# Optimization experiments

Hardware: AMD Instinct MI355X
Metric: run time of the kernel (lower is better)

Reference implementation:

```python
import jax, jax.numpy as jnp
import numpy as np

QMIN, QMAX = -128, 127  # int8 range

def setup_inputs() -> dict:
    key = jax.random.key(0)
    k1, k2, k3 = jax.random.split(key, 3)
    B, S, DIN, DOUT = 8, 2048, 4096, 4096
    x = jax.random.normal(k1, (B, S, DIN), dtype=jnp.float32)
    weight = jax.random.normal(k2, (DOUT, DIN), dtype=jnp.float32) * 0.02
    bias = jax.random.normal(k3, (DOUT,), dtype=jnp.float32) * 0.01
    # per-tensor asymmetric activation qparams (as produced by a calibrated observer)
    act_scale = jnp.float32(0.05)
    act_zero_point = jnp.int32(3)
    # per-output-channel symmetric weight scales (block_size = (1, in_features))
    weight_scale = jnp.max(jnp.abs(weight), axis=1) / 127.0  # [DOUT]
    return {"x": x, "weight": weight, "bias": bias,
            "act_scale": act_scale, "act_zero_point": act_zero_point,
            "weight_scale": weight_scale}

def reference(x, weight, bias, act_scale, act_zero_point, weight_scale):
    # 1) quantize activations: per-tensor asymmetric int8
    qx = jnp.clip(jnp.round(x / act_scale) + act_zero_point, QMIN, QMAX).astype(jnp.int8)
    # 2) quantize weight: per-output-channel symmetric int8 (zero_point = 0)
    qw = jnp.clip(jnp.round(weight / weight_scale[:, None]), QMIN, QMAX).astype(jnp.int8)
    acc = jnp.einsum('bsk,nk->bsn',
                     qx.astype(jnp.int32) - act_zero_point.astype(jnp.int32),
                     qw.astype(jnp.int32))  # [B, S, DOUT] int32
    # 4) dequantize: combined scale = act_scale * weight_scale[n], then bias
    out = acc.astype(jnp.float32) * (act_scale * weight_scale) + bias
    return out
```

## Files before the change

### kernel.cpp

```cpp
#include <hip/hip_runtime.h>
#include <cstdint>

#define M_DIM 16384
#define N_DIM 4096
#define K_DIM 4096

#define BM 256
#define BN 256
#define BK 128

typedef __attribute__((ext_vector_type(4))) int int32x4;
typedef __attribute__((ext_vector_type(4))) float f32x4;

#define GLLD16(g, l)                                              \
  __builtin_amdgcn_global_load_lds(                               \
      (const __attribute__((address_space(1))) void*)(g),         \
      (__attribute__((address_space(3))) void*)(l), 16, 0, 0)

__global__ void quant_x_kernel(const float* __restrict__ x,
                               const float* __restrict__ sp,
                               const int* __restrict__ zpp,
                               int8_t* __restrict__ qx) {
  const float s = sp[0];
  const int zp = zpp[0];
  const size_t b = (size_t)blockIdx.x * 1024;
  const f32x4* x4 = (const f32x4*)x;
  unsigned* q4 = (unsigned*)qx;
#pragma unroll
  for (int i = 0; i < 4; i++) {
    const size_t idx = b + (size_t)i * 256 + threadIdx.x;
    f32x4 v = __builtin_nontemporal_load(&x4[idx]);
    int q0 = min(127, max(-128, (int)rintf(v[0] / s) + zp));
    int q1 = min(127, max(-128, (int)rintf(v[1] / s) + zp));
    int q2 = min(127, max(-128, (int)rintf(v[2] / s) + zp));
    int q3 = min(127, max(-128, (int)rintf(v[3] / s) + zp));
    q4[idx] = (unsigned)(q0 & 255) | ((unsigned)(q1 & 255) << 8) |
              ((unsigned)(q2 & 255) << 16) | ((unsigned)(q3 & 255) << 24);
  }
}

__global__ void quant_w_kernel(const float* __restrict__ w,
                               const float* __restrict__ wscale,
                               const float* __restrict__ bias,
                               const float* __restrict__ sp,
                               const int* __restrict__ zpp,
                               int8_t* __restrict__ qw,
                               float* __restrict__ cs,
                               float* __restrict__ off) {
  const int n = blockIdx.x;
  const float ws = wscale[n];
  const float s = sp[0];
  const int zp = zpp[0];
  const f32x4* wr = (const f32x4*)(w + (size_t)n * K_DIM);
  unsigned* qr = (unsigned*)(qw + (size_t)n * K_DIM);
  int sum = 0;
#pragma unroll
  for (int it = 0; it < K_DIM / (256 * 4); it++) {
    const int idx = it * 256 + threadIdx.x;
    f32x4 v = __builtin_nontemporal_load(&wr[idx]);
    int q0 = min(127, max(-128, (int)rintf(v[0] / ws)));
    int q1 = min(127, max(-128, (int)rintf(v[1] / ws)));
    int q2 = min(127, max(-128, (int)rintf(v[2] / ws)));
    int q3 = min(127, max(-128, (int)rintf(v[3] / ws)));
    sum += q0 + q1 + q2 + q3;
    qr[idx] = (unsigned)(q0 & 255) | ((unsigned)(q1 & 255) << 8) |
              ((unsigned)(q2 & 255) << 16) | ((unsigned)(q3 & 255) << 24);
  }
  __shared__ int red[4];
#pragma unroll
  for (int o = 32; o > 0; o >>= 1) sum += __shfl_down(sum, o, 64);
  if ((threadIdx.x & 63) == 0) red[threadIdx.x >> 6] = sum;
  __syncthreads();
  if (threadIdx.x == 0) {
    const int tot = red[0] + red[1] + red[2] + red[3];
    const float c = s * ws;
    cs[n] = c;
    off[n] = bias[n] - (float)(zp * tot) * c;
  }
}

__global__ __launch_bounds__(512, 2) void gemm_i8(
    const int8_t* __restrict__ qx, const int8_t* __restrict__ qw,
    const float* __restrict__ cs, const float* __restrict__ off,
    float* __restrict__ out) {
  __shared__ __align__(16) int8_t lds[131072];

  const int tid = threadIdx.x;
  const int lane = tid & 63;
  const int wave = tid >> 6;
  const int wm = wave >> 2;
  const int wn = wave & 3;

  const int bid = blockIdx.x;
  const int swz = (bid & 7) * 128 + (bid >> 3);
  const int n0 = (swz & 15) * BN;
  const int m0 = (swz >> 4) * BM;

  int32x4 acc[8][4] = {};
  int32x4 af[8], bf0[4], bf1[4];

  const int scol = ((lane & 7) ^ ((lane >> 3) & 7)) * 16;
  const int8_t* pA[2][2];
  const int8_t* pB[2][2];
#pragma unroll
  for (int h = 0; h < 2; h++)
#pragma unroll
    for (int j = 0; j < 2; j++) {
      const int r = h * 128 + (wave * 2 + j) * 8 + (lane >> 3);
      const int ga = ((r >> 6) & 1) * 128 + (r >> 7) * 64 + (r & 63);
      const int gb = ((r >> 5) & 3) * 64 + (r >> 7) * 32 + (r & 31);
      pA[h][j] = qx + (size_t)(m0 + ga) * K_DIM + scol;
      pB[h][j] = qw + (size_t)(n0 + gb) * K_DIM + scol;
    }

  const int fr = lane & 15;
  const int quad = lane >> 4;
  int aoffs[8], boffs[4];
#pragma unroll
  for (int mtl = 0; mtl < 4; mtl++)
#pragma unroll
    for (int ks = 0; ks < 2; ks++) {
      const int r = wm * 64 + mtl * 16 + fr;
      const int c = (ks * 4 + quad) ^ (fr & 7);
      aoffs[mtl * 2 + ks] = r * 128 + c * 16;
    }
#pragma unroll
  for (int ntl = 0; ntl < 2; ntl++)
#pragma unroll
    for (int ks = 0; ks < 2; ks++) {
      const int r = wn * 32 + ntl * 16 + fr;
      const int c = (ks * 4 + quad) ^ (fr & 7);
      boffs[ntl * 2 + ks] = r * 128 + c * 16;
    }

#define STAGE(rbase, h, P, kb)                                          \
  do {                                                                  \
    GLLD16(P[h][0] + (kb), lds + (rbase) + (h) * 16384 + wave * 2048);  \
    GLLD16(P[h][1] + (kb),                                              \
           lds + (rbase) + (h) * 16384 + wave * 2048 + 1024);           \
  } while (0)

#define LDA(buf, h)                                                     \
  do {                                                                  \
    _Pragma("unroll") for (int q = 0; q < 8; q++) af[q] =               \
        *(const int32x4*)(lds + (buf) * 65536 + (h) * 16384 + aoffs[q]); \
  } while (0)

#define LDB(buf, g, BF)                                                 \
  do {                                                                  \
    _Pragma("unroll") for (int q = 0; q < 4; q++) BF[q] =               \
        *(const int32x4*)(lds + (buf) * 65536 + 32768 + (g) * 16384 +   \
                          boffs[q]);                                    \
  } while (0)

#define MM(h, g, BF)                                                       \
  do {                                                                    \
    _Pragma("unroll") for (int mtl = 0; mtl < 4; mtl++)                   \
        _Pragma("unroll") for (int ntl = 0; ntl < 2; ntl++) {             \
      acc[(h)*4 + mtl][(g)*2 + ntl] = __builtin_amdgcn_mfma_i32_16x16x64_i8( \
          BF[ntl * 2 + 0], af[mtl * 2 + 0], acc[(h)*4 + mtl][(g)*2 + ntl], \
          0, 0, 0);                                                        \
      acc[(h)*4 + mtl][(g)*2 + ntl] = __builtin_amdgcn_mfma_i32_16x16x64_i8( \
          BF[ntl * 2 + 1], af[mtl * 2 + 1], acc[(h)*4 + mtl][(g)*2 + ntl], \
          0, 0, 0);                                                        \
    }                                                                      \
  } while (0)

#define BAR() __builtin_amdgcn_s_barrier()
#define WAITLGKM() asm volatile("s_waitcnt lgkmcnt(0)" ::: "memory")
#define VM6() asm volatile("s_waitcnt vmcnt(6)" ::: "memory")
#define PRIO(x) __builtin_amdgcn_s_setprio(x)

  STAGE(0, 0, pA, 0);
  STAGE(0, 1, pA, 0);
  STAGE(32768, 0, pB, 0);
  STAGE(32768, 1, pB, 0);
  STAGE(65536, 0, pA, 128);
  STAGE(98304, 0, pB, 128);
  STAGE(98304, 1, pB, 128);
  VM6();
  BAR();

  for (int i = 0; i < K_DIM / (2 * BK); i++) {
    const int kb1 = ((2 * i + 1) << 7) & (K_DIM - 1);
    const int kb2 = ((2 * i + 2) << 7) & (K_DIM - 1);
    const int kb3 = ((2 * i + 3) << 7) & (K_DIM - 1);
    LDA(0, 0);
    LDB(0, 0, bf0);
    STAGE(65536, 1, pA, kb1);
    BAR(); WAITLGKM(); PRIO(1); MM(0, 0, bf0); PRIO(0); BAR();
    LDB(0, 1, bf1);
    STAGE(0, 0, pA, kb2);
    BAR(); WAITLGKM(); PRIO(1); MM(0, 1, bf1); PRIO(0); BAR();
    LDA(0, 1);
    STAGE(32768, 0, pB, kb2);
    BAR(); WAITLGKM(); PRIO(1); MM(1, 1, bf1); PRIO(0); BAR();
    STAGE(32768, 1, pB, kb2);
    VM6();
    BAR(); PRIO(1); MM(1, 0, bf0); PRIO(0); BAR();
    LDA(1, 0);
    LDB(1, 0, bf0);
    STAGE(0, 1, pA, kb2);
    BAR(); WAITLGKM(); PRIO(1); MM(0, 0, bf0); PRIO(0); BAR();
    LDB(1, 1, bf1);
    STAGE(65536, 0, pA, kb3);
    BAR(); WAITLGKM(); PRIO(1); MM(0, 1, bf1); PRIO(0); BAR();
    LDA(1, 1);
    STAGE(98304, 0, pB, kb3);
    BAR(); WAITLGKM(); PRIO(1); MM(1, 1, bf1); PRIO(0); BAR();
    STAGE(98304, 1, pB, kb3);
    VM6();
    BAR(); PRIO(1); MM(1, 0, bf0); PRIO(0); BAR();
  }

#pragma unroll
  for (int nt = 0; nt < 4; nt++) {
    const int colb = n0 + wn * 64 + nt * 16 + quad * 4;
    const f32x4 c4 = *(const f32x4*)(cs + colb);
    const f32x4 o4 = *(const f32x4*)(off + colb);
#pragma unroll
    for (int mt = 0; mt < 8; mt++) {
      const int row = m0 + wm * 128 + mt * 16 + fr;
      f32x4 v;
      v[0] = (float)acc[mt][nt][0] * c4[0] + o4[0];
      v[1] = (float)acc[mt][nt][1] * c4[1] + o4[1];
      v[2] = (float)acc[mt][nt][2] * c4[2] + o4[2];
      v[3] = (float)acc[mt][nt][3] * c4[3] + o4[3];
      __builtin_nontemporal_store(
          v, (f32x4*)(out + (size_t)row * N_DIM + colb));
    }
  }
#undef STAGE
#undef LDA
#undef LDB
#undef MM
#undef BAR
#undef WAITLGKM
#undef VM6
#undef PRIO
}

extern "C" void kernel_launch(void* const* d_in, const int* in_sizes, int n_in,
                              void* d_out, int out_size, void* d_ws,
                              size_t ws_size, hipStream_t stream) {
  const float* x = (const float*)d_in[0];
  const float* w = (const float*)d_in[1];
  const float* bias = (const float*)d_in[2];
  const float* act_scale = (const float*)d_in[3];
  const int* zp = (const int*)d_in[4];
  const float* wscale = (const float*)d_in[5];
  float* out = (float*)d_out;

  int8_t* qx = (int8_t*)d_ws;
  int8_t* qw = qx + (size_t)M_DIM * K_DIM;
  float* cs = (float*)(qw + (size_t)N_DIM * K_DIM);
  float* off = cs + N_DIM;

  quant_x_kernel<<<16384, 256, 0, stream>>>(x, act_scale, zp, qx);
  quant_w_kernel<<<N_DIM, 256, 0, stream>>>(w, wscale, bias, act_scale, zp,
                                            qw, cs, off);
  gemm_i8<<<dim3((M_DIM / BM) * (N_DIM / BN)), 512, 0, stream>>>(qx, qw, cs,
                                                                 off, out);
}
```

Baseline: 666.2 us.

## Fuse quant kernels and restructure GEMM to stream B from global

```diff
diff --git a/kernel.cpp b/kernel.cpp
--- a/kernel.cpp
+++ b/kernel.cpp
@@ -17,65 +17,64 @@
       (const __attribute__((address_space(1))) void*)(g),         \
       (__attribute__((address_space(3))) void*)(l), 16, 0, 0)
 
-__global__ void quant_x_kernel(const float* __restrict__ x,
-                               const float* __restrict__ sp,
-                               const int* __restrict__ zpp,
-                               int8_t* __restrict__ qx) {
-  const float s = sp[0];
-  const int zp = zpp[0];
-  const size_t b = (size_t)blockIdx.x * 1024;
-  const f32x4* x4 = (const f32x4*)x;
-  unsigned* q4 = (unsigned*)qx;
-#pragma unroll
-  for (int i = 0; i < 4; i++) {
-    const size_t idx = b + (size_t)i * 256 + threadIdx.x;
-    f32x4 v = __builtin_nontemporal_load(&x4[idx]);
-    int q0 = min(127, max(-128, (int)rintf(v[0] / s) + zp));
-    int q1 = min(127, max(-128, (int)rintf(v[1] / s) + zp));
-    int q2 = min(127, max(-128, (int)rintf(v[2] / s) + zp));
-    int q3 = min(127, max(-128, (int)rintf(v[3] / s) + zp));
-    q4[idx] = (unsigned)(q0 & 255) | ((unsigned)(q1 & 255) << 8) |
-              ((unsigned)(q2 & 255) << 16) | ((unsigned)(q3 & 255) << 24);
-  }
-}
-
-__global__ void quant_w_kernel(const float* __restrict__ w,
-                               const float* __restrict__ wscale,
-                               const float* __restrict__ bias,
-                               const float* __restrict__ sp,
-                               const int* __restrict__ zpp,
-                               int8_t* __restrict__ qw,
-                               float* __restrict__ cs,
-                               float* __restrict__ off) {
-  const int n = blockIdx.x;
-  const float ws = wscale[n];
-  const float s = sp[0];
-  const int zp = zpp[0];
-  const f32x4* wr = (const f32x4*)(w + (size_t)n * K_DIM);
-  unsigned* qr = (unsigned*)(qw + (size_t)n * K_DIM);
-  int sum = 0;
-#pragma unroll
-  for (int it = 0; it < K_DIM / (256 * 4); it++) {
-    const int idx = it * 256 + threadIdx.x;
-    f32x4 v = __builtin_nontemporal_load(&wr[idx]);
-    int q0 = min(127, max(-128, (int)rintf(v[0] / ws)));
-    int q1 = min(127, max(-128, (int)rintf(v[1] / ws)));
-    int q2 = min(127, max(-128, (int)rintf(v[2] / ws)));
-    int q3 = min(127, max(-128, (int)rintf(v[3] / ws)));
-    sum += q0 + q1 + q2 + q3;
-    qr[idx] = (unsigned)(q0 & 255) | ((unsigned)(q1 & 255) << 8) |
-              ((unsigned)(q2 & 255) << 16) | ((unsigned)(q3 & 255) << 24);
-  }
+__global__ void quant_fused(const float* __restrict__ x,
+                            const float* __restrict__ w,
+                            const float* __restrict__ wscale,
+                            const float* __restrict__ bias,
+                            const float* __restrict__ sp,
+                            const int* __restrict__ zpp,
+                            int8_t* __restrict__ qx,
+                            int8_t* __restrict__ qw,
+                            float* __restrict__ cs,
+                            float* __restrict__ off) {
   __shared__ int red[4];
-#pragma unroll
-  for (int o = 32; o > 0; o >>= 1) sum += __shfl_down(sum, o, 64);
-  if ((threadIdx.x & 63) == 0) red[threadIdx.x >> 6] = sum;
-  __syncthreads();
-  if (threadIdx.x == 0) {
-    const int tot = red[0] + red[1] + red[2] + red[3];
-    const float c = s * ws;
-    cs[n] = c;
-    off[n] = bias[n] - (float)(zp * tot) * c;
+  if (blockIdx.x < 16384) {
+    const float s = sp[0];
+    const int zp = zpp[0];
+    const size_t b = (size_t)blockIdx.x * 1024;
+    const f32x4* x4 = (const f32x4*)x;
+    unsigned* q4 = (unsigned*)qx;
+#pragma unroll
+    for (int i = 0; i < 4; i++) {
+      const size_t idx = b + (size_t)i * 256 + threadIdx.x;
+      f32x4 v = __builtin_nontemporal_load(&x4[idx]);
+      int q0 = min(127, max(-128, (int)rintf(v[0] / s) + zp));
+      int q1 = min(127, max(-128, (int)rintf(v[1] / s) + zp));
+      int q2 = min(127, max(-128, (int)rintf(v[2] / s) + zp));
+      int q3 = min(127, max(-128, (int)rintf(v[3] / s) + zp));
+      q4[idx] = (unsigned)(q0 & 255) | ((unsigned)(q1 & 255) << 8) |
+                ((unsigned)(q2 & 255) << 16) | ((unsigned)(q3 & 255) << 24);
+    }
+  } else {
+    const int n = blockIdx.x - 16384;
+    const float ws = wscale[n];
+    const float s = sp[0];
+    const int zp = zpp[0];
+    const f32x4* wr = (const f32x4*)(w + (size_t)n * K_DIM);
+    unsigned* qr = (unsigned*)(qw + (size_t)n * K_DIM);
+    int sum = 0;
+#pragma unroll
+    for (int it = 0; it < K_DIM / (256 * 4); it++) {
+      const int idx = it * 256 + threadIdx.x;
+      f32x4 v = __builtin_nontemporal_load(&wr[idx]);
+      int q0 = min(127, max(-128, (int)rintf(v[0] / ws)));
+      int q1 = min(127, max(-128, (int)rintf(v[1] / ws)));
+      int q2 = min(127, max(-128, (int)rintf(v[2] / ws)));
+      int q3 = min(127, max(-128, (int)rintf(v[3] / ws)));
+      sum += q0 + q1 + q2 + q3;
+      qr[idx] = (unsigned)(q0 & 255) | ((unsigned)(q1 & 255) << 8) |
+                ((unsigned)(q2 & 255) << 16) | ((unsigned)(q3 & 255) << 24);
+    }
+#pragma unroll
+    for (int o = 32; o > 0; o >>= 1) sum += __shfl_down(sum, o, 64);
+    if ((threadIdx.x & 63) == 0) red[threadIdx.x >> 6] = sum;
+    __syncthreads();
+    if (threadIdx.x == 0) {
+      const int tot = red[0] + red[1] + red[2] + red[3];
+      const float c = s * ws;
+      cs[n] = c;
+      off[n] = bias[n] - (float)(zp * tot) * c;
+    }
   }
 }
 
@@ -83,144 +82,120 @@
     const int8_t* __restrict__ qx, const int8_t* __restrict__ qw,
     const float* __restrict__ cs, const float* __restrict__ off,
     float* __restrict__ out) {
-  __shared__ __align__(16) int8_t lds[131072];
+  __shared__ __align__(16) int8_t lds[98304];
 
   const int tid = threadIdx.x;
   const int lane = tid & 63;
   const int wave = tid >> 6;
-  const int wm = wave >> 2;
-  const int wn = wave & 3;
+  const int wm = wave >> 1;
+  const int wn = wave & 1;
 
   const int bid = blockIdx.x;
   const int swz = (bid & 7) * 128 + (bid >> 3);
   const int n0 = (swz & 15) * BN;
   const int m0 = (swz >> 4) * BM;
 
-  int32x4 acc[8][4] = {};
-  int32x4 af[8], bf0[4], bf1[4];
-
-  const int scol = ((lane & 7) ^ ((lane >> 3) & 7)) * 16;
-  const int8_t* pA[2][2];
-  const int8_t* pB[2][2];
-#pragma unroll
-  for (int h = 0; h < 2; h++)
-#pragma unroll
-    for (int j = 0; j < 2; j++) {
-      const int r = h * 128 + (wave * 2 + j) * 8 + (lane >> 3);
-      const int ga = ((r >> 6) & 1) * 128 + (r >> 7) * 64 + (r & 63);
-      const int gb = ((r >> 5) & 3) * 64 + (r >> 7) * 32 + (r & 31);
-      pA[h][j] = qx + (size_t)(m0 + ga) * K_DIM + scol;
-      pB[h][j] = qw + (size_t)(n0 + gb) * K_DIM + scol;
-    }
+  int32x4 acc[4][8] = {};
+  int32x4 afA[8], afB[8], bf0[4], bf1[4];
 
   const int fr = lane & 15;
   const int quad = lane >> 4;
-  int aoffs[8], boffs[4];
-#pragma unroll
-  for (int mtl = 0; mtl < 4; mtl++)
-#pragma unroll
-    for (int ks = 0; ks < 2; ks++) {
-      const int r = wm * 64 + mtl * 16 + fr;
-      const int c = (ks * 4 + quad) ^ (fr & 7);
-      aoffs[mtl * 2 + ks] = r * 128 + c * 16;
-    }
-#pragma unroll
-  for (int ntl = 0; ntl < 2; ntl++)
-#pragma unroll
-    for (int ks = 0; ks < 2; ks++) {
-      const int r = wn * 32 + ntl * 16 + fr;
-      const int c = (ks * 4 + quad) ^ (fr & 7);
-      boffs[ntl * 2 + ks] = r * 128 + c * 16;
-    }
-
-#define STAGE(rbase, h, P, kb)                                          \
-  do {                                                                  \
-    GLLD16(P[h][0] + (kb), lds + (rbase) + (h) * 16384 + wave * 2048);  \
-    GLLD16(P[h][1] + (kb),                                              \
-           lds + (rbase) + (h) * 16384 + wave * 2048 + 1024);           \
-  } while (0)
-
-#define LDA(buf, h)                                                     \
-  do {                                                                  \
-    _Pragma("unroll") for (int q = 0; q < 8; q++) af[q] =               \
-        *(const int32x4*)(lds + (buf) * 65536 + (h) * 16384 + aoffs[q]); \
-  } while (0)
-
-#define LDB(buf, g, BF)                                                 \
-  do {                                                                  \
-    _Pragma("unroll") for (int q = 0; q < 4; q++) BF[q] =               \
-        *(const int32x4*)(lds + (buf) * 65536 + 32768 + (g) * 16384 +   \
-                          boffs[q]);                                    \
-  } while (0)
-
-#define MM(h, g, BF)                                                       \
+
+  const int8_t* pSA = qx + (size_t)(m0 + wave * 16 + (lane >> 3)) * K_DIM +
+                      (((lane & 7) ^ ((lane >> 3) & 7)) * 16);
+  const int dBase = wave * 2048 + lane * 16;
+
+  const int fb2 = (fr >> 2) & 1;
+  const int aBase = (wm * 64 + fr) * 128 + ((quad ^ (fr & 3)) * 16);
+  const int aB0 = aBase + fb2 * 64;
+  const int aB1 = aBase + (1 ^ fb2) * 64;
+
+  const int8_t* qwB = qw + (size_t)n0 * K_DIM;
+  const unsigned vB = (unsigned)((wn * 128 + fr) * K_DIM + quad * 16);
+
+#define STAGE(offS, ktv)                                                  \
+  do {                                                                    \
+    GLLD16(pSA + (ktv), lds + (offS) + dBase);                            \
+    GLLD16(pSA + (ktv) + 32768, lds + (offS) + dBase + 1024);             \
+    GLLD16(pSA + (ktv) + 524288, lds + (offS) + dBase + 16384);           \
+    GLLD16(pSA + (ktv) + 557056, lds + (offS) + dBase + 17408);           \
+  } while (0)
+
+#define LDA(offS, AF)                                                     \
+  do {                                                                    \
+    _Pragma("unroll") for (int mtl = 0; mtl < 4; mtl++) {                 \
+      AF[mtl * 2 + 0] = *(const int32x4*)(lds + (offS) + aB0 + mtl * 2048); \
+      AF[mtl * 2 + 1] = *(const int32x4*)(lds + (offS) + aB1 + mtl * 2048); \
+    }                                                                     \
+  } while (0)
+
+#define LDBG(g, ktv, BF)                                                  \
+  do {                                                                    \
+    _Pragma("unroll") for (int ntl = 0; ntl < 2; ntl++)                   \
+        _Pragma("unroll") for (int ks = 0; ks < 2; ks++)                  \
+            BF[ntl * 2 + ks] = *(const int32x4*)(qwB +                    \
+                (size_t)(vB + ntl * 65536u + (g) * 131072u + ks * 64u +   \
+                         (unsigned)(ktv)));                               \
+  } while (0)
+
+#define MM(g, BF, AF)                                                      \
   do {                                                                    \
     _Pragma("unroll") for (int mtl = 0; mtl < 4; mtl++)                   \
         _Pragma("unroll") for (int ntl = 0; ntl < 2; ntl++) {             \
-      acc[(h)*4 + mtl][(g)*2 + ntl] = __builtin_amdgcn_mfma_i32_16x16x64_i8( \
-          BF[ntl * 2 + 0], af[mtl * 2 + 0], acc[(h)*4 + mtl][(g)*2 + ntl], \
-          0, 0, 0);                                                        \
-      acc[(h)*4 + mtl][(g)*2 + ntl] = __builtin_amdgcn_mfma_i32_16x16x64_i8( \
-          BF[ntl * 2 + 1], af[mtl * 2 + 1], acc[(h)*4 + mtl][(g)*2 + ntl], \
-          0, 0, 0);                                                        \
+      acc[mtl][(g)*2 + ntl] = __builtin_amdgcn_mfma_i32_16x16x64_i8(      \
+          BF[ntl * 2 + 0], AF[mtl * 2 + 0], acc[mtl][(g)*2 + ntl], 0, 0, 0); \
+      acc[mtl][(g)*2 + ntl] = __builtin_amdgcn_mfma_i32_16x16x64_i8(      \
+          BF[ntl * 2 + 1], AF[mtl * 2 + 1], acc[mtl][(g)*2 + ntl], 0, 0, 0); \
     }                                                                      \
   } while (0)
 
 #define BAR() __builtin_amdgcn_s_barrier()
-#define WAITLGKM() asm volatile("s_waitcnt lgkmcnt(0)" ::: "memory")
-#define VM6() asm volatile("s_waitcnt vmcnt(6)" ::: "memory")
+#define VM4() asm volatile("s_waitcnt vmcnt(4)" ::: "memory")
 #define PRIO(x) __builtin_amdgcn_s_setprio(x)
 
-  STAGE(0, 0, pA, 0);
-  STAGE(0, 1, pA, 0);
-  STAGE(32768, 0, pB, 0);
-  STAGE(32768, 1, pB, 0);
-  STAGE(65536, 0, pA, 128);
-  STAGE(98304, 0, pB, 128);
-  STAGE(98304, 1, pB, 128);
-  VM6();
+#define BODY(AF_USE, AF_LD)                                               \
+  do {                                                                    \
+    STAGE(oS, (kt + 256) & (K_DIM - 1));                                  \
+    LDBG(1, kt, bf1);                                                     \
+    PRIO(1); MM(0, bf0, AF_USE); PRIO(0);                                 \
+    LDA(oN, AF_LD);                                                       \
+    LDBG(2, kt, bf0);                                                     \
+    PRIO(1); MM(1, bf1, AF_USE); PRIO(0);                                 \
+    LDBG(3, kt, bf1);                                                     \
+    PRIO(1); MM(2, bf0, AF_USE); PRIO(0);                                 \
+    LDBG(0, (kt + 128) & (K_DIM - 1), bf0);                               \
+    PRIO(1); MM(3, bf1, AF_USE); PRIO(0);                                 \
+    VM4();                                                                \
+    BAR();                                                                \
+    {                                                                     \
+      const int tmp = oC; oC = oN; oN = oS; oS = tmp;                     \
+    }                                                                     \
+    kt = (kt + 128) & (K_DIM - 1);                                        \
+  } while (0)
+
+  int oC = 0, oN = 32768, oS = 65536;
+  int kt = 0;
+
+  STAGE(0, 0);
+  STAGE(32768, 128);
+  LDBG(0, 0, bf0);
+  VM4();
   BAR();
-
-  for (int i = 0; i < K_DIM / (2 * BK); i++) {
-    const int kb1 = ((2 * i + 1) << 7) & (K_DIM - 1);
-    const int kb2 = ((2 * i + 2) << 7) & (K_DIM - 1);
-    const int kb3 = ((2 * i + 3) << 7) & (K_DIM - 1);
-    LDA(0, 0);
-    LDB(0, 0, bf0);
-    STAGE(65536, 1, pA, kb1);
-    BAR(); WAITLGKM(); PRIO(1); MM(0, 0, bf0); PRIO(0); BAR();
-    LDB(0, 1, bf1);
-    STAGE(0, 0, pA, kb2);
-    BAR(); WAITLGKM(); PRIO(1); MM(0, 1, bf1); PRIO(0); BAR();
-    LDA(0, 1);
-    STAGE(32768, 0, pB, kb2);
-    BAR(); WAITLGKM(); PRIO(1); MM(1, 1, bf1); PRIO(0); BAR();
-    STAGE(32768, 1, pB, kb2);
-    VM6();
-    BAR(); PRIO(1); MM(1, 0, bf0); PRIO(0); BAR();
-    LDA(1, 0);
-    LDB(1, 0, bf0);
-    STAGE(0, 1, pA, kb2);
-    BAR(); WAITLGKM(); PRIO(1); MM(0, 0, bf0); PRIO(0); BAR();
-    LDB(1, 1, bf1);
-    STAGE(65536, 0, pA, kb3);
-    BAR(); WAITLGKM(); PRIO(1); MM(0, 1, bf1); PRIO(0); BAR();
-    LDA(1, 1);
-    STAGE(98304, 0, pB, kb3);
-    BAR(); WAITLGKM(); PRIO(1); MM(1, 1, bf1); PRIO(0); BAR();
-    STAGE(98304, 1, pB, kb3);
-    VM6();
-    BAR(); PRIO(1); MM(1, 0, bf0); PRIO(0); BAR();
+  LDA(0, afA);
+
+  for (int t = 0; t < K_DIM / BK; t += 2) {
+    BODY(afA, afB);
+    BODY(afB, afA);
   }
 
 #pragma unroll
-  for (int nt = 0; nt < 4; nt++) {
-    const int colb = n0 + wn * 64 + nt * 16 + quad * 4;
+  for (int nt = 0; nt < 8; nt++) {
+    const int colb = n0 + wn * 128 + nt * 16 + quad * 4;
     const f32x4 c4 = *(const f32x4*)(cs + colb);
     const f32x4 o4 = *(const f32x4*)(off + colb);
 #pragma unroll
-    for (int mt = 0; mt < 8; mt++) {
-      const int row = m0 + wm * 128 + mt * 16 + fr;
+    for (int mt = 0; mt < 4; mt++) {
+      const int row = m0 + wm * 64 + mt * 16 + fr;
       f32x4 v;
       v[0] = (float)acc[mt][nt][0] * c4[0] + o4[0];
       v[1] = (float)acc[mt][nt][1] * c4[1] + o4[1];
@@ -232,12 +207,12 @@
   }
 #undef STAGE
 #undef LDA
-#undef LDB
+#undef LDBG
 #undef MM
 #undef BAR
-#undef WAITLGKM
-#undef VM6
+#undef VM4
 #undef PRIO
+#undef BODY
 }
 
 extern "C" void kernel_launch(void* const* d_in, const int* in_sizes, int n_in,
@@ -256,9 +231,9 @@
   float* cs = (float*)(qw + (size_t)N_DIM * K_DIM);
   float* off = cs + N_DIM;
 
-  quant_x_kernel<<<16384, 256, 0, stream>>>(x, act_scale, zp, qx);
-  quant_w_kernel<<<N_DIM, 256, 0, stream>>>(w, wscale, bias, act_scale, zp,
-                                            qw, cs, off);
+  quant_fused<<<16384 + N_DIM, 256, 0, stream>>>(x, w, wscale, bias,
+                                                 act_scale, zp, qx, qw, cs,
+                                                 off);
   gemm_i8<<<dim3((M_DIM / BM) * (N_DIM / BN)), 512, 0, stream>>>(qx, qw, cs,
                                                                  off, out);
 }
```

After: 961.9 us. +44.4%, slower.

## Fuse quantization kernels and restructure GEMM main loop with fewer barriers

Applied to the files above, without the earlier changes.

```diff
diff --git a/kernel.cpp b/kernel.cpp
--- a/kernel.cpp
+++ b/kernel.cpp
@@ -17,65 +17,65 @@
       (const __attribute__((address_space(1))) void*)(g),         \
       (__attribute__((address_space(3))) void*)(l), 16, 0, 0)
 
-__global__ void quant_x_kernel(const float* __restrict__ x,
-                               const float* __restrict__ sp,
-                               const int* __restrict__ zpp,
-                               int8_t* __restrict__ qx) {
-  const float s = sp[0];
-  const int zp = zpp[0];
-  const size_t b = (size_t)blockIdx.x * 1024;
-  const f32x4* x4 = (const f32x4*)x;
-  unsigned* q4 = (unsigned*)qx;
-#pragma unroll
-  for (int i = 0; i < 4; i++) {
-    const size_t idx = b + (size_t)i * 256 + threadIdx.x;
-    f32x4 v = __builtin_nontemporal_load(&x4[idx]);
-    int q0 = min(127, max(-128, (int)rintf(v[0] / s) + zp));
-    int q1 = min(127, max(-128, (int)rintf(v[1] / s) + zp));
-    int q2 = min(127, max(-128, (int)rintf(v[2] / s) + zp));
-    int q3 = min(127, max(-128, (int)rintf(v[3] / s) + zp));
-    q4[idx] = (unsigned)(q0 & 255) | ((unsigned)(q1 & 255) << 8) |
-              ((unsigned)(q2 & 255) << 16) | ((unsigned)(q3 & 255) << 24);
-  }
-}
-
-__global__ void quant_w_kernel(const float* __restrict__ w,
-                               const float* __restrict__ wscale,
-                               const float* __restrict__ bias,
-                               const float* __restrict__ sp,
-                               const int* __restrict__ zpp,
-                               int8_t* __restrict__ qw,
-                               float* __restrict__ cs,
-                               float* __restrict__ off) {
-  const int n = blockIdx.x;
-  const float ws = wscale[n];
-  const float s = sp[0];
-  const int zp = zpp[0];
-  const f32x4* wr = (const f32x4*)(w + (size_t)n * K_DIM);
-  unsigned* qr = (unsigned*)(qw + (size_t)n * K_DIM);
-  int sum = 0;
-#pragma unroll
-  for (int it = 0; it < K_DIM / (256 * 4); it++) {
-    const int idx = it * 256 + threadIdx.x;
-    f32x4 v = __builtin_nontemporal_load(&wr[idx]);
-    int q0 = min(127, max(-128, (int)rintf(v[0] / ws)));
-    int q1 = min(127, max(-128, (int)rintf(v[1] / ws)));
-    int q2 = min(127, max(-128, (int)rintf(v[2] / ws)));
-    int q3 = min(127, max(-128, (int)rintf(v[3] / ws)));
-    sum += q0 + q1 + q2 + q3;
-    qr[idx] = (unsigned)(q0 & 255) | ((unsigned)(q1 & 255) << 8) |
-              ((unsigned)(q2 & 255) << 16) | ((unsigned)(q3 & 255) << 24);
-  }
+__global__ void quant_fused(const float* __restrict__ x,
+                            const float* __restrict__ w,
+                            const float* __restrict__ wscale,
+                            const float* __restrict__ bias,
+                            const float* __restrict__ sp,
+                            const int* __restrict__ zpp,
+                            int8_t* __restrict__ qx,
+                            int8_t* __restrict__ qw,
+                            float* __restrict__ cs,
+                            float* __restrict__ off) {
   __shared__ int red[4];
-#pragma unroll
-  for (int o = 32; o > 0; o >>= 1) sum += __shfl_down(sum, o, 64);
-  if ((threadIdx.x & 63) == 0) red[threadIdx.x >> 6] = sum;
-  __syncthreads();
-  if (threadIdx.x == 0) {
-    const int tot = red[0] + red[1] + red[2] + red[3];
-    const float c = s * ws;
-    cs[n] = c;
-    off[n] = bias[n] - (float)(zp * tot) * c;
+  if (blockIdx.x < 16384) {
+    const float rs = 1.0f / sp[0];
+    const int zp = zpp[0];
+    const size_t b = (size_t)blockIdx.x * 1024;
+    const f32x4* x4 = (const f32x4*)x;
+    unsigned* q4 = (unsigned*)qx;
+#pragma unroll
+    for (int i = 0; i < 4; i++) {
+      const size_t idx = b + (size_t)i * 256 + threadIdx.x;
+      f32x4 v = __builtin_nontemporal_load(&x4[idx]);
+      int q0 = min(127, max(-128, (int)rintf(v[0] * rs) + zp));
+      int q1 = min(127, max(-128, (int)rintf(v[1] * rs) + zp));
+      int q2 = min(127, max(-128, (int)rintf(v[2] * rs) + zp));
+      int q3 = min(127, max(-128, (int)rintf(v[3] * rs) + zp));
+      q4[idx] = (unsigned)(q0 & 255) | ((unsigned)(q1 & 255) << 8) |
+                ((unsigned)(q2 & 255) << 16) | ((unsigned)(q3 & 255) << 24);
+    }
+  } else {
+    const int n = blockIdx.x - 16384;
+    const float ws = wscale[n];
+    const float rws = 1.0f / ws;
+    const float s = sp[0];
+    const int zp = zpp[0];
+    const f32x4* wr = (const f32x4*)(w + (size_t)n * K_DIM);
+    unsigned* qr = (unsigned*)(qw + (size_t)n * K_DIM);
+    int sum = 0;
+#pragma unroll
+    for (int it = 0; it < K_DIM / (256 * 4); it++) {
+      const int idx = it * 256 + threadIdx.x;
+      f32x4 v = __builtin_nontemporal_load(&wr[idx]);
+      int q0 = min(127, max(-128, (int)rintf(v[0] * rws)));
+      int q1 = min(127, max(-128, (int)rintf(v[1] * rws)));
+      int q2 = min(127, max(-128, (int)rintf(v[2] * rws)));
+      int q3 = min(127, max(-128, (int)rintf(v[3] * rws)));
+      sum += q0 + q1 + q2 + q3;
+      qr[idx] = (unsigned)(q0 & 255) | ((unsigned)(q1 & 255) << 8) |
+                ((unsigned)(q2 & 255) << 16) | ((unsigned)(q3 & 255) << 24);
+    }
+#pragma unroll
+    for (int o = 32; o > 0; o >>= 1) sum += __shfl_down(sum, o, 64);
+    if ((threadIdx.x & 63) == 0) red[threadIdx.x >> 6] = sum;
+    __syncthreads();
+    if (threadIdx.x == 0) {
+      const int tot = red[0] + red[1] + red[2] + red[3];
+      const float c = s * ws;
+      cs[n] = c;
+      off[n] = bias[n] - (float)(zp * tot) * c;
+    }
   }
 }
 
@@ -168,7 +168,7 @@
 
 #define BAR() __builtin_amdgcn_s_barrier()
 #define WAITLGKM() asm volatile("s_waitcnt lgkmcnt(0)" ::: "memory")
-#define VM6() asm volatile("s_waitcnt vmcnt(6)" ::: "memory")
+#define VM8() asm volatile("s_waitcnt vmcnt(8)" ::: "memory")
 #define PRIO(x) __builtin_amdgcn_s_setprio(x)
 
   STAGE(0, 0, pA, 0);
@@ -176,9 +176,10 @@
   STAGE(32768, 0, pB, 0);
   STAGE(32768, 1, pB, 0);
   STAGE(65536, 0, pA, 128);
+  STAGE(65536, 1, pA, 128);
   STAGE(98304, 0, pB, 128);
   STAGE(98304, 1, pB, 128);
-  VM6();
+  VM8();
   BAR();
 
   for (int i = 0; i < K_DIM / (2 * BK); i++) {
@@ -187,30 +188,40 @@
     const int kb3 = ((2 * i + 3) << 7) & (K_DIM - 1);
     LDA(0, 0);
     LDB(0, 0, bf0);
+    LDB(0, 1, bf1);
+    WAITLGKM();
+    PRIO(1); MM(0, 0, bf0); PRIO(0);
     STAGE(65536, 1, pA, kb1);
-    BAR(); WAITLGKM(); PRIO(1); MM(0, 0, bf0); PRIO(0); BAR();
-    LDB(0, 1, bf1);
+    PRIO(1); MM(0, 1, bf1); PRIO(0);
+    VM8();
+    BAR();
+    LDA(0, 1);
+    WAITLGKM();
+    PRIO(1); MM(1, 1, bf1); PRIO(0);
     STAGE(0, 0, pA, kb2);
-    BAR(); WAITLGKM(); PRIO(1); MM(0, 1, bf1); PRIO(0); BAR();
-    LDA(0, 1);
     STAGE(32768, 0, pB, kb2);
-    BAR(); WAITLGKM(); PRIO(1); MM(1, 1, bf1); PRIO(0); BAR();
     STAGE(32768, 1, pB, kb2);
-    VM6();
-    BAR(); PRIO(1); MM(1, 0, bf0); PRIO(0); BAR();
+    PRIO(1); MM(1, 0, bf0); PRIO(0);
+    VM8();
+    BAR();
     LDA(1, 0);
     LDB(1, 0, bf0);
+    LDB(1, 1, bf1);
+    WAITLGKM();
+    PRIO(1); MM(0, 0, bf0); PRIO(0);
     STAGE(0, 1, pA, kb2);
-    BAR(); WAITLGKM(); PRIO(1); MM(0, 0, bf0); PRIO(0); BAR();
-    LDB(1, 1, bf1);
+    PRIO(1); MM(0, 1, bf1); PRIO(0);
+    VM8();
+    BAR();
+    LDA(1, 1);
+    WAITLGKM();
+    PRIO(1); MM(1, 1, bf1); PRIO(0);
     STAGE(65536, 0, pA, kb3);
-    BAR(); WAITLGKM(); PRIO(1); MM(0, 1, bf1); PRIO(0); BAR();
-    LDA(1, 1);
     STAGE(98304, 0, pB, kb3);
-    BAR(); WAITLGKM(); PRIO(1); MM(1, 1, bf1); PRIO(0); BAR();
     STAGE(98304, 1, pB, kb3);
-    VM6();
-    BAR(); PRIO(1); MM(1, 0, bf0); PRIO(0); BAR();
+    PRIO(1); MM(1, 0, bf0); PRIO(0);
+    VM8();
+    BAR();
   }
 
 #pragma unroll
@@ -236,7 +247,7 @@
 #undef MM
 #undef BAR
 #undef WAITLGKM
-#undef VM6
+#undef VM8
 #undef PRIO
 }
 
@@ -256,9 +267,9 @@
   float* cs = (float*)(qw + (size_t)N_DIM * K_DIM);
   float* off = cs + N_DIM;
 
-  quant_x_kernel<<<16384, 256, 0, stream>>>(x, act_scale, zp, qx);
-  quant_w_kernel<<<N_DIM, 256, 0, stream>>>(w, wscale, bias, act_scale, zp,
-                                            qw, cs, off);
+  quant_fused<<<16384 + N_DIM, 256, 0, stream>>>(x, w, wscale, bias,
+                                                 act_scale, zp, qx, qw, cs,
+                                                 off);
   gemm_i8<<<dim3((M_DIM / BM) * (N_DIM / BN)), 512, 0, stream>>>(qx, qw, cs,
                                                                  off, out);
 }
```

Result: no change. 661.3 us (-0.7%).
